# Performance work log

Hardware: AMD Instinct MI355X
Metric: run time of the kernel (lower is better)

## Reference

```python
import jax, jax.numpy as jnp
import numpy as np

N_NODES = 100000
N_EDGES = 3200000
D_IN = 256
HID = 256
N_CLASSES = 40


def setup_inputs() -> dict:
    key = jax.random.key(0)
    k1, k2, k3, k4 = jax.random.split(key, 4)
    x = jax.random.normal(k1, (N_NODES, D_IN), dtype=jnp.float32)
    edge_index = jax.random.randint(k2, (2, N_EDGES), 0, N_NODES, dtype=jnp.int64)
    W1 = jax.random.normal(k3, (D_IN, HID), dtype=jnp.float32) * (1.0 / np.sqrt(D_IN))
    b1 = jnp.zeros((HID,), dtype=jnp.float32)
    W2 = jax.random.normal(k4, (HID, N_CLASSES), dtype=jnp.float32) * (1.0 / np.sqrt(HID))
    b2 = jnp.zeros((N_CLASSES,), dtype=jnp.float32)
    return {"x": x, "edge_index": edge_index, "W1": W1, "b1": b1, "W2": W2, "b2": b2}


def reference(x, edge_index, W1, b1, W2, b2):
    N = x.shape[0]
    loops = jnp.arange(N, dtype=edge_index.dtype)
    # gcn_norm: add self-loops, symmetric normalization D^-1/2 (A+I) D^-1/2
    src = jnp.concatenate([edge_index[0], loops])  # [E+N]
    dst = jnp.concatenate([edge_index[1], loops])
    ew = jnp.ones(src.shape[0], dtype=x.dtype)
    deg = jax.ops.segment_sum(ew, dst, num_segments=N)  # degree at target nodes
    dinv = jnp.where(deg > 0, jax.lax.rsqrt(deg), 0.0).astype(x.dtype)
    norm = dinv[src] * dinv[dst]  # [E+N]

    def propagate(h):
        # out[dst] += norm * h[src]  (SpMM via gather + segment scatter-add)
        return jax.ops.segment_sum(norm[:, None] * h[src], dst, num_segments=N)

    h = propagate(x) @ W1 + b1   # SGConv k=1 + Linear
    h = jax.nn.relu(h)
    h = propagate(h) @ W2 + b2
    return jax.nn.log_softmax(h, axis=1)
```

## Files before the change

kernel.cpp:

```cpp
#include <hip/hip_runtime.h>
#include <hip/hip_bf16.h>

#define N_NODES 100000
#define N_EDGES 3200000
#define D_IN 256
#define HID 256
#define NC 40
#define NBUCK 391
#define CHUNK 8192
#define BIN1_BLOCKS ((N_EDGES + CHUNK - 1) / CHUNK)
#define BCAP 16384
#define NPADE (NBUCK * BCAP)

typedef unsigned short u16;
typedef unsigned int u32;
typedef __attribute__((ext_vector_type(8))) short bf16x8;
typedef __attribute__((ext_vector_type(4))) float f32x4;
typedef __attribute__((ext_vector_type(2))) float f32x2;

static __device__ __forceinline__ float bf2f(u16 u) {
  union { unsigned int i; float f; } c; c.i = ((unsigned int)u) << 16; return c.f;
}
static __device__ __forceinline__ u16 f2bf(float f) {
  union { float f; unsigned int i; } c; c.f = f;
  unsigned int x = c.i;
  x += 0x7fffu + ((x >> 16) & 1u);
  return (u16)(x >> 16);
}

__global__ void k_zero(int* __restrict__ gcur) {
  int i = blockIdx.x * 256 + threadIdx.x;
  if (i < NBUCK) gcur[i] = i * BCAP;
}

__global__ __launch_bounds__(1024) void k_bin1(const int* __restrict__ ei,
    int* __restrict__ gcur, u32* __restrict__ binned) {
  __shared__ int cnt[NBUCK];
  __shared__ int base[NBUCK];
  int t = threadIdx.x;
  int e0 = blockIdx.x * CHUNK;
  for (int j = t; j < NBUCK; j += 1024) cnt[j] = 0;
  __syncthreads();
  for (int j = 0; j < CHUNK / 1024; ++j) {
    int e = e0 + j * 1024 + t;
    if (e < N_EDGES) {
      unsigned d = (unsigned)ei[N_EDGES + e];
      if (d < N_NODES) atomicAdd(&cnt[d >> 8], 1);
    }
  }
  __syncthreads();
  for (int j = t; j < NBUCK; j += 1024)
    base[j] = cnt[j] ? atomicAdd(&gcur[j], cnt[j]) : 0;
  __syncthreads();
  for (int j = 0; j < CHUNK / 1024; ++j) {
    int e = e0 + j * 1024 + t;
    if (e < N_EDGES) {
      unsigned s = (unsigned)ei[e];
      unsigned d = (unsigned)ei[N_EDGES + e];
      if (s < N_NODES && d < N_NODES) {
        int b = d >> 8;
        int pos = atomicAdd(&base[b], 1);
        if ((unsigned)pos < NPADE)
          binned[pos] = ((d & 255u) << 17) | s;
      }
    }
  }
}

__global__ __launch_bounds__(1024) void k_bin2(const u32* __restrict__ binned,
    const int* __restrict__ gcur, int* __restrict__ rp, int* __restrict__ re,
    float* __restrict__ dinv, int* __restrict__ ed) {
  __shared__ int cnt[256];
  __shared__ int s[256];
  __shared__ int cur[256];
  int b = blockIdx.x, t = threadIdx.x;
  int start = b * BCAP, end = gcur[b];
  if (t < 256) cnt[t] = 0;
  __syncthreads();
  for (int i = start + t; i < end; i += 1024)
    atomicAdd(&cnt[binned[i] >> 17], 1);
  __syncthreads();
  int v = (t < 256) ? cnt[t] : 0;
  if (t < 256) s[t] = v;
  __syncthreads();
  for (int off = 1; off < 256; off <<= 1) {
    int add = (t >= off && t < 256) ? s[t - off] : 0;
    __syncthreads();
    if (t < 256) s[t] += add;
    __syncthreads();
  }
  if (t < 256) {
    int excl = s[t] - v;
    int n = b * 256 + t;
    if (n < N_NODES) {
      rp[n] = start + excl;
      re[n] = start + excl + v;
      dinv[n] = rsqrtf((float)v + 1.0f);
    }
    cur[t] = start + excl;
  }
  __syncthreads();
  for (int i = start + t; i < end; i += 1024) {
    u32 rec = binned[i];
    int pos = atomicAdd(&cur[rec >> 17], 1);
    if ((unsigned)pos < NPADE) ed[pos] = (int)(rec & 0x1FFFFu);
  }
}

__global__ void k_w1t(const float* __restrict__ W1, u16* __restrict__ w1t) {
  int n = blockIdx.x, k = threadIdx.x;
  w1t[n * 256 + k] = f2bf(W1[k * 256 + n]);
}
__global__ void k_w2t(const float* __restrict__ W2, u16* __restrict__ w2t) {
  int n = blockIdx.x, k = threadIdx.x;
  w2t[n * 256 + k] = (n < NC) ? f2bf(W2[k * NC + n]) : (u16)0;
}

__global__ __launch_bounds__(256) void k_gemm1(const float* __restrict__ x,
    const u16* __restrict__ w1t, const float* __restrict__ dinv,
    unsigned char* __restrict__ y) {
  __shared__ char smem[20480];
  short* sA = (short*)smem;
  short* sB = (short*)(smem + 10240);
  float* sdinv = (float*)(smem + 18432);
  int tid = threadIdx.x;
  int wave = tid >> 6, lane = tid & 63;
  int lq = lane >> 4, lr = lane & 15;
  int wm = (wave >> 1) * 64, wn = (wave & 1) * 64;
  int row0 = blockIdx.y * 128;
  int col0 = blockIdx.x * 128;
  int sr = tid >> 1;
  int sh = (tid & 1) * 16;
  int arow = row0 + sr;
  bool aval = arow < N_NODES;
  const float* axf = x + (size_t)arow * 256 + sh;
  const u16* bx = w1t + (size_t)(col0 + sr) * 256 + sh;
  f32x4 acc[4][4] = {};
  for (int k0 = 0; k0 < 256; k0 += 32) {
    float4 f0 = {}, f1 = {}, f2 = {}, f3 = {};
    if (aval) {
      f0 = *(const float4*)(axf + k0);
      f1 = *(const float4*)(axf + k0 + 4);
      f2 = *(const float4*)(axf + k0 + 8);
      f3 = *(const float4*)(axf + k0 + 12);
    }
    uint4 vb0 = *(const uint4*)(bx + k0);
    uint4 vb1 = *(const uint4*)(bx + k0 + 8);
    uint4 pa0, pa1;
    pa0.x = (u32)f2bf(f0.x) | ((u32)f2bf(f0.y) << 16);
    pa0.y = (u32)f2bf(f0.z) | ((u32)f2bf(f0.w) << 16);
    pa0.z = (u32)f2bf(f1.x) | ((u32)f2bf(f1.y) << 16);
    pa0.w = (u32)f2bf(f1.z) | ((u32)f2bf(f1.w) << 16);
    pa1.x = (u32)f2bf(f2.x) | ((u32)f2bf(f2.y) << 16);
    pa1.y = (u32)f2bf(f2.z) | ((u32)f2bf(f2.w) << 16);
    pa1.z = (u32)f2bf(f3.x) | ((u32)f2bf(f3.y) << 16);
    pa1.w = (u32)f2bf(f3.z) | ((u32)f2bf(f3.w) << 16);
    __syncthreads();
    *(uint4*)&sA[sr * 40 + sh] = pa0;
    *(uint4*)&sA[sr * 40 + sh + 8] = pa1;
    *(uint4*)&sB[sr * 40 + sh] = vb0;
    *(uint4*)&sB[sr * 40 + sh + 8] = vb1;
    __syncthreads();
    bf16x8 af[4], bfr[4];
#pragma unroll
    for (int mt = 0; mt < 4; ++mt)
      af[mt] = *(const bf16x8*)&sA[(wm + mt * 16 + lr) * 40 + lq * 8];
#pragma unroll
    for (int nt = 0; nt < 4; ++nt)
      bfr[nt] = *(const bf16x8*)&sB[(wn + nt * 16 + lr) * 40 + lq * 8];
#pragma unroll
    for (int mt = 0; mt < 4; ++mt)
#pragma unroll
      for (int nt = 0; nt < 4; ++nt)
        acc[mt][nt] = __builtin_amdgcn_mfma_f32_16x16x32_bf16(
            af[mt], bfr[nt], acc[mt][nt], 0, 0, 0);
  }
  __syncthreads();
  if (tid < 128) {
    int rr = row0 + tid;
    sdinv[tid] = (rr < N_NODES) ? dinv[rr] : 0.f;
  }
  __syncthreads();
#pragma unroll
  for (int mt = 0; mt < 4; ++mt)
#pragma unroll
    for (int nt = 0; nt < 4; ++nt) {
      int c = wn + nt * 16 + lr;
#pragma unroll
      for (int i = 0; i < 4; ++i) {
        int r = wm + mt * 16 + lq * 4 + i;
        float sv = sdinv[r] * acc[mt][nt][i];
        int pk = __builtin_amdgcn_cvt_pk_fp8_f32(sv, sv, 0, false);
        smem[r * 144 + c] = (char)(pk & 0xFF);
      }
    }
  __syncthreads();
  if (aval) {
    unsigned char* dst = y + (size_t)arow * 256 + col0 + (tid & 1) * 64;
    const char* srcp = smem + sr * 144 + (tid & 1) * 64;
#pragma unroll
    for (int j = 0; j < 4; ++j)
      ((uint4*)dst)[j] = *(const uint4*)(srcp + j * 16);
  }
}

#define ACC8(U) do { \
    acc[0] += __builtin_amdgcn_cvt_pk_f32_fp8((U).x, false); \
    acc[1] += __builtin_amdgcn_cvt_pk_f32_fp8((U).x, true);  \
    acc[2] += __builtin_amdgcn_cvt_pk_f32_fp8((U).y, false); \
    acc[3] += __builtin_amdgcn_cvt_pk_f32_fp8((U).y, true);  \
    acc[4] += __builtin_amdgcn_cvt_pk_f32_fp8((U).z, false); \
    acc[5] += __builtin_amdgcn_cvt_pk_f32_fp8((U).z, true);  \
    acc[6] += __builtin_amdgcn_cvt_pk_f32_fp8((U).w, false); \
    acc[7] += __builtin_amdgcn_cvt_pk_f32_fp8((U).w, true);  \
  } while (0)

__global__ __launch_bounds__(256) void k_spmm1(const uint4* __restrict__ y16,
    const int* __restrict__ ed, const int* __restrict__ rp,
    const int* __restrict__ re, const float* __restrict__ dinv,
    const float* __restrict__ b1, u16* __restrict__ h1, int row0) {
  int lane = threadIdx.x & 63;
  int row = row0 + (blockIdx.x << 2) + (threadIdx.x >> 6);
  int g = lane >> 4, p = lane & 15;
  float di = dinv[row];
  uint4 sv = y16[(size_t)row * 16 + p];
  f32x2 acc[8];
  f32x2 z2 = {0.f, 0.f};
  if (g == 0) {
    acc[0] = __builtin_amdgcn_cvt_pk_f32_fp8(sv.x, false);
    acc[1] = __builtin_amdgcn_cvt_pk_f32_fp8(sv.x, true);
    acc[2] = __builtin_amdgcn_cvt_pk_f32_fp8(sv.y, false);
    acc[3] = __builtin_amdgcn_cvt_pk_f32_fp8(sv.y, true);
    acc[4] = __builtin_amdgcn_cvt_pk_f32_fp8(sv.z, false);
    acc[5] = __builtin_amdgcn_cvt_pk_f32_fp8(sv.z, true);
    acc[6] = __builtin_amdgcn_cvt_pk_f32_fp8(sv.w, false);
    acc[7] = __builtin_amdgcn_cvt_pk_f32_fp8(sv.w, true);
  } else {
#pragma unroll
    for (int i = 0; i < 8; ++i) acc[i] = z2;
  }
  int e = rp[row], e1 = re[row];
  if (e + 16 <= e1) {
    int s0 = ed[e + g], s1 = ed[e + 4 + g];
    int s2 = ed[e + 8 + g], s3 = ed[e + 12 + g];
    while (true) {
      uint4 u0 = y16[(size_t)s0 * 16 + p];
      uint4 u1 = y16[(size_t)s1 * 16 + p];
      uint4 u2 = y16[(size_t)s2 * 16 + p];
      uint4 u3 = y16[(size_t)s3 * 16 + p];
      e += 16;
      bool more = (e + 16 <= e1);
      if (more) {
        s0 = ed[e + g]; s1 = ed[e + 4 + g];
        s2 = ed[e + 8 + g]; s3 = ed[e + 12 + g];
      }
      ACC8(u0);
      ACC8(u1);
      ACC8(u2);
      ACC8(u3);
      if (!more) break;
    }
  }
  for (; e + 4 <= e1; e += 4) {
    int s0 = ed[e + g];
    uint4 u0 = y16[(size_t)s0 * 16 + p];
    ACC8(u0);
  }
  int rem = e1 - e;
  if (rem > 0) {
    int s0 = ed[e + (g < rem ? g : 0)];
    uint4 u0 = y16[(size_t)s0 * 16 + p];
    if (g < rem) ACC8(u0);
  }
#pragma unroll
  for (int i = 0; i < 8; ++i) {
    acc[i].x += __shfl_xor(acc[i].x, 16);
    acc[i].y += __shfl_xor(acc[i].y, 16);
    acc[i].x += __shfl_xor(acc[i].x, 32);
    acc[i].y += __shfl_xor(acc[i].y, 32);
  }
  if (g == 0) {
    const float4* bb4 = (const float4*)(b1 + p * 16);
    u16 o[16];
#pragma unroll
    for (int i = 0; i < 4; ++i) {
      float4 bb = bb4[i];
      float a0 = fmaxf(di * acc[2 * i].x + bb.x, 0.f);
      float a1 = fmaxf(di * acc[2 * i].y + bb.y, 0.f);
      float a2 = fmaxf(di * acc[2 * i + 1].x + bb.z, 0.f);
      float a3 = fmaxf(di * acc[2 * i + 1].y + bb.w, 0.f);
      o[4 * i + 0] = f2bf(a0);
      o[4 * i + 1] = f2bf(a1);
      o[4 * i + 2] = f2bf(a2);
      o[4 * i + 3] = f2bf(a3);
    }
    u16* dst = h1 + (size_t)row * HID + p * 16;
    *(uint4*)dst = *(const uint4*)&o[0];
    *(uint4*)(dst + 8) = *(const uint4*)&o[8];
  }
}

__global__ __launch_bounds__(256) void k_gemm2(const u16* __restrict__ h1,
    const u16* __restrict__ w2t, const float* __restrict__ dinv,
    u16* __restrict__ zbp) {
  __shared__ char smem[16384];
  short* sA = (short*)smem;
  short* sB = (short*)(smem + 10240);
  float* sdinv = (float*)(smem + 14336);
  u16* sC = (u16*)smem;
  int tid = threadIdx.x;
  int wave = tid >> 6, lane = tid & 63;
  int lq = lane >> 4, lr = lane & 15;
  int wm = wave * 32;
  int row0 = blockIdx.x * 128;
  int sr = tid >> 1;
  int sh = (tid & 1) * 16;
  int arow = row0 + sr;
  bool aval = arow < N_NODES;
  const u16* ax = h1 + (size_t)arow * 256 + sh;
  int br = tid >> 1;
  const u16* bx = w2t + (size_t)br * 256 + sh;
  if (tid < 128) {
    int rr = row0 + tid;
    sdinv[tid] = (rr < N_NODES) ? dinv[rr] : 0.f;
  }
  f32x4 acc[2][3] = {};
  for (int k0 = 0; k0 < 256; k0 += 32) {
    uint4 a0 = {}, a1 = {};
    if (aval) {
      a0 = *(const uint4*)(ax + k0);
      a1 = *(const uint4*)(ax + k0 + 8);
    }
    uint4 b0 = {}, b1v = {};
    if (tid < 96) {
      b0 = *(const uint4*)(bx + k0);
      b1v = *(const uint4*)(bx + k0 + 8);
    }
    __syncthreads();
    *(uint4*)&sA[sr * 40 + sh] = a0;
    *(uint4*)&sA[sr * 40 + sh + 8] = a1;
    if (tid < 96) {
      *(uint4*)&sB[br * 40 + sh] = b0;
      *(uint4*)&sB[br * 40 + sh + 8] = b1v;
    }
    __syncthreads();
    bf16x8 af[2], bfr[3];
#pragma unroll
    for (int mt = 0; mt < 2; ++mt)
      af[mt] = *(const bf16x8*)&sA[(wm + mt * 16 + lr) * 40 + lq * 8];
#pragma unroll
    for (int nt = 0; nt < 3; ++nt)
      bfr[nt] = *(const bf16x8*)&sB[(nt * 16 + lr) * 40 + lq * 8];
#pragma unroll
    for (int mt = 0; mt < 2; ++mt)
#pragma unroll
      for (int nt = 0; nt < 3; ++nt)
        acc[mt][nt] = __builtin_amdgcn_mfma_f32_16x16x32_bf16(
            af[mt], bfr[nt], acc[mt][nt], 0, 0, 0);
  }
  __syncthreads();
#pragma unroll
  for (int mt = 0; mt < 2; ++mt)
#pragma unroll
    for (int nt = 0; nt < 3; ++nt) {
      int c = nt * 16 + lr;
#pragma unroll
      for (int i = 0; i < 4; ++i) {
        int r = wm + mt * 16 + lq * 4 + i;
        sC[r * 56 + c] = f2bf(sdinv[r] * acc[mt][nt][i]);
      }
    }
  __syncthreads();
  if (tid < 128) {
    int orow = row0 + tid;
    if (orow < N_NODES) {
      u16* dst = zbp + (size_t)orow * 64;
#pragma unroll
      for (int j = 0; j < 6; ++j)
        ((uint4*)dst)[j] = *(const uint4*)&sC[tid * 56 + j * 8];
      uint4 z = {};
      ((uint4*)dst)[6] = z;
      ((uint4*)dst)[7] = z;
    }
  }
}

#define ZACC(U) do { \
    acc[0] += __uint_as_float((U).x << 16); \
    acc[1] += __uint_as_float((U).x & 0xFFFF0000u); \
    acc[2] += __uint_as_float((U).y << 16); \
    acc[3] += __uint_as_float((U).y & 0xFFFF0000u); \
    acc[4] += __uint_as_float((U).z << 16); \
    acc[5] += __uint_as_float((U).z & 0xFFFF0000u); \
    acc[6] += __uint_as_float((U).w << 16); \
    acc[7] += __uint_as_float((U).w & 0xFFFF0000u); \
  } while (0)

__global__ __launch_bounds__(256) void k_spmm2(const uint4* __restrict__ zb4,
    const int* __restrict__ ed, const int* __restrict__ rp,
    const int* __restrict__ re, const float* __restrict__ dinv,
    const float* __restrict__ b2, float* __restrict__ out, int row0) {
  int lane = threadIdx.x & 63;
  int row = row0 + (blockIdx.x << 2) + (threadIdx.x >> 6);
  int g = lane >> 3, p = lane & 7;
  float di = dinv[row];
  float acc[8];
  uint4 sv = zb4[(size_t)row * 8 + p];
  if (g == 0) {
    acc[0] = __uint_as_float(sv.x << 16);
    acc[1] = __uint_as_float(sv.x & 0xFFFF0000u);
    acc[2] = __uint_as_float(sv.y << 16);
    acc[3] = __uint_as_float(sv.y & 0xFFFF0000u);
    acc[4] = __uint_as_float(sv.z << 16);
    acc[5] = __uint_as_float(sv.z & 0xFFFF0000u);
    acc[6] = __uint_as_float(sv.w << 16);
    acc[7] = __uint_as_float(sv.w & 0xFFFF0000u);
  } else {
#pragma unroll
    for (int i = 0; i < 8; ++i) acc[i] = 0.f;
  }
  int e = rp[row], e1 = re[row];
  if (e + 32 <= e1) {
    int s0 = ed[e + g], s1 = ed[e + 8 + g];
    int s2 = ed[e + 16 + g], s3 = ed[e + 24 + g];
    while (true) {
      uint4 u0 = zb4[(size_t)s0 * 8 + p];
      uint4 u1 = zb4[(size_t)s1 * 8 + p];
      uint4 u2 = zb4[(size_t)s2 * 8 + p];
      uint4 u3 = zb4[(size_t)s3 * 8 + p];
      e += 32;
      bool more = (e + 32 <= e1);
      if (more) {
        s0 = ed[e + g]; s1 = ed[e + 8 + g];
        s2 = ed[e + 16 + g]; s3 = ed[e + 24 + g];
      }
      ZACC(u0);
      ZACC(u1);
      ZACC(u2);
      ZACC(u3);
      if (!more) break;
    }
  }
  for (; e + 8 <= e1; e += 8) {
    int s0 = ed[e + g];
    uint4 u0 = zb4[(size_t)s0 * 8 + p];
    ZACC(u0);
  }
  int rem = e1 - e;
  if (g < rem) {
    int s0 = ed[e + g];
    uint4 u0 = zb4[(size_t)s0 * 8 + p];
    ZACC(u0);
  }
#pragma unroll
  for (int i = 0; i < 8; ++i) {
    acc[i] += __shfl_xor(acc[i], 8);
    acc[i] += __shfl_xor(acc[i], 16);
    acc[i] += __shfl_xor(acc[i], 32);
  }
  bool valid = p < 5;
  float val[8];
  if (valid) {
    float4 bb0 = *(const float4*)(b2 + p * 8);
    float4 bb1 = *(const float4*)(b2 + p * 8 + 4);
    val[0] = di * acc[0] + bb0.x;
    val[1] = di * acc[1] + bb0.y;
    val[2] = di * acc[2] + bb0.z;
    val[3] = di * acc[3] + bb0.w;
    val[4] = di * acc[4] + bb1.x;
    val[5] = di * acc[5] + bb1.y;
    val[6] = di * acc[6] + bb1.z;
    val[7] = di * acc[7] + bb1.w;
  } else {
#pragma unroll
    for (int i = 0; i < 8; ++i) val[i] = 0.f;
  }
  float mv = -3.0e38f;
  if (valid) {
#pragma unroll
    for (int i = 0; i < 8; ++i) mv = fmaxf(mv, val[i]);
  }
  mv = fmaxf(mv, __shfl_xor(mv, 1));
  mv = fmaxf(mv, __shfl_xor(mv, 2));
  mv = fmaxf(mv, __shfl_xor(mv, 4));
  float sum = 0.f;
  if (valid) {
#pragma unroll
    for (int i = 0; i < 8; ++i) sum += expf(val[i] - mv);
  }
  sum += __shfl_xor(sum, 1);
  sum += __shfl_xor(sum, 2);
  sum += __shfl_xor(sum, 4);
  float ls = logf(sum);
  if (g == 0 && valid) {
    float4 o0, o1;
    o0.x = val[0] - mv - ls; o0.y = val[1] - mv - ls;
    o0.z = val[2] - mv - ls; o0.w = val[3] - mv - ls;
    o1.x = val[4] - mv - ls; o1.y = val[5] - mv - ls;
    o1.z = val[6] - mv - ls; o1.w = val[7] - mv - ls;
    float* dst = out + (size_t)row * NC + p * 8;
    *(float4*)dst = o0;
    *(float4*)(dst + 4) = o1;
  }
}

extern "C" void kernel_launch(void* const* d_in, const int* in_sizes, int n_in,
                              void* d_out, int out_size, void* d_ws, size_t ws_size,
                              hipStream_t stream) {
  const float* x  = (const float*)d_in[0];
  const int*   ei = (const int*)d_in[1];
  const float* W1 = (const float*)d_in[2];
  const float* b1 = (const float*)d_in[3];
  const float* W2 = (const float*)d_in[4];
  const float* b2 = (const float*)d_in[5];
  float* out = (float*)d_out;

  char* ws = (char*)d_ws;
  size_t off = 0;
  auto alloc = [&](size_t bytes) {
    char* p = ws + off;
    off = (off + bytes + 255) & ~(size_t)255;
    return p;
  };
  int*   gcur   = (int*)  alloc((size_t)NBUCK * 4);
  int*   rp     = (int*)  alloc((size_t)N_NODES * 4);
  int*   re     = (int*)  alloc((size_t)N_NODES * 4);
  float* dinv   = (float*)alloc((size_t)N_NODES * 4);
  u32*   binned = (u32*)  alloc((size_t)NPADE * 4);
  int*   ed     = (int*)  alloc((size_t)NPADE * 4);
  unsigned char* y = (unsigned char*)alloc((size_t)N_NODES * 256);
  u16*   w1t    = (u16*)  alloc((size_t)256 * 256 * 2);
  u16*   w2t    = (u16*)  alloc((size_t)48 * 256 * 2);
  u16*   h1     = (u16*)  alloc((size_t)N_NODES * HID * 2);
  u16*   zbp    = (u16*)  alloc((size_t)N_NODES * 64 * 2);

  k_zero<<<2, 256, 0, stream>>>(gcur);
  k_bin1<<<BIN1_BLOCKS, 1024, 0, stream>>>(ei, gcur, binned);
  k_bin2<<<NBUCK, 1024, 0, stream>>>(binned, gcur, rp, re, dinv, ed);
  k_w1t<<<256, 256, 0, stream>>>(W1, w1t);
  k_w2t<<<48, 256, 0, stream>>>(W2, w2t);
  k_gemm1<<<dim3(2, (N_NODES + 127) / 128), 256, 0, stream>>>(x, w1t, dinv, y);
  k_spmm1<<<N_NODES / 8, 256, 0, stream>>>((const uint4*)y, ed, rp, re, dinv, b1, h1, 0);
  k_spmm1<<<N_NODES / 8, 256, 0, stream>>>((const uint4*)y, ed, rp, re, dinv, b1, h1, N_NODES / 2);
  k_gemm2<<<(N_NODES + 127) / 128, 256, 0, stream>>>(h1, w2t, dinv, zbp);
  k_spmm2<<<N_NODES / 8, 256, 0, stream>>>((const uint4*)zbp, ed, rp, re, dinv, b2, out, 0);
  k_spmm2<<<N_NODES / 8, 256, 0, stream>>>((const uint4*)zbp, ed, rp, re, dinv, b2, out, N_NODES / 2);
}
```

Baseline: 481.3 us.

## Double-buffer LDS in gemm1 with XOR-swizzled layout and packed bf16 conversion

Restructures the first GEMM's main loop to use two LDS buffers, so the next K-slice is loaded and staged while MFMAs run on the current one. This cuts the loop to one barrier per step instead of two. It also replaces the padded row stride with an XOR swizzle to avoid bank conflicts, and uses a packed float2-to-bf16 conversion intrinsic. The dinv load is hoisted before the loop. In exchange, LDS use grows to about 33KB per block, which may reduce occupancy, and GEMM1 is likely only part of the total runtime.

```diff
diff --git a/kernel.cpp b/kernel.cpp
--- a/kernel.cpp
+++ b/kernel.cpp
@@ -26,6 +26,10 @@
   unsigned int x = c.i;
   x += 0x7fffu + ((x >> 16) & 1u);
   return (u16)(x >> 16);
+}
+static __device__ __forceinline__ u32 pkbf(float a, float b) {
+  __hip_bfloat162 t = __float22bfloat162_rn(make_float2(a, b));
+  union { __hip_bfloat162 h; u32 u; } c; c.h = t; return c.u;
 }
 
 __global__ void k_zero(int* __restrict__ gcur) {
@@ -119,10 +123,8 @@
 __global__ __launch_bounds__(256) void k_gemm1(const float* __restrict__ x,
     const u16* __restrict__ w1t, const float* __restrict__ dinv,
     unsigned char* __restrict__ y) {
-  __shared__ char smem[20480];
-  short* sA = (short*)smem;
-  short* sB = (short*)(smem + 10240);
-  float* sdinv = (float*)(smem + 18432);
+  __shared__ char smem[33280];
+  float* sdinv = (float*)(smem + 32768);
   int tid = threadIdx.x;
   int wave = tid >> 6, lane = tid & 63;
   int lq = lane >> 4, lr = lane & 15;
@@ -130,13 +132,27 @@
   int row0 = blockIdx.y * 128;
   int col0 = blockIdx.x * 128;
   int sr = tid >> 1;
-  int sh = (tid & 1) * 16;
+  int h = tid & 1;
+  int sh = h * 16;
   int arow = row0 + sr;
   bool aval = arow < N_NODES;
   const float* axf = x + (size_t)arow * 256 + sh;
   const u16* bx = w1t + (size_t)(col0 + sr) * 256 + sh;
-  f32x4 acc[4][4] = {};
-  for (int k0 = 0; k0 < 256; k0 += 32) {
+  if (tid < 128) {
+    int rr = row0 + tid;
+    sdinv[tid] = (rr < N_NODES) ? dinv[rr] : 0.f;
+  }
+  int wsw0 = sr * 32 + (((2 * h)     ^ ((sr >> 1) & 3)) * 8);
+  int wsw1 = sr * 32 + (((2 * h + 1) ^ ((sr >> 1) & 3)) * 8);
+  int rdo[4], rdb[4];
+#pragma unroll
+  for (int mt = 0; mt < 4; ++mt) {
+    int Ra = wm + mt * 16 + lr;
+    int Rb = wn + mt * 16 + lr;
+    rdo[mt] = Ra * 32 + ((lq ^ ((Ra >> 1) & 3)) * 8);
+    rdb[mt] = Rb * 32 + ((lq ^ ((Rb >> 1) & 3)) * 8);
+  }
+  auto stage = [&](int k0, int boff) {
     float4 f0 = {}, f1 = {}, f2 = {}, f3 = {};
     if (aval) {
       f0 = *(const float4*)(axf + k0);
@@ -147,40 +163,44 @@
     uint4 vb0 = *(const uint4*)(bx + k0);
     uint4 vb1 = *(const uint4*)(bx + k0 + 8);
     uint4 pa0, pa1;
-    pa0.x = (u32)f2bf(f0.x) | ((u32)f2bf(f0.y) << 16);
-    pa0.y = (u32)f2bf(f0.z) | ((u32)f2bf(f0.w) << 16);
-    pa0.z = (u32)f2bf(f1.x) | ((u32)f2bf(f1.y) << 16);
-    pa0.w = (u32)f2bf(f1.z) | ((u32)f2bf(f1.w) << 16);
-    pa1.x = (u32)f2bf(f2.x) | ((u32)f2bf(f2.y) << 16);
-    pa1.y = (u32)f2bf(f2.z) | ((u32)f2bf(f2.w) << 16);
-    pa1.z = (u32)f2bf(f3.x) | ((u32)f2bf(f3.y) << 16);
-    pa1.w = (u32)f2bf(f3.z) | ((u32)f2bf(f3.w) << 16);
-    __syncthreads();
-    *(uint4*)&sA[sr * 40 + sh] = pa0;
-    *(uint4*)&sA[sr * 40 + sh + 8] = pa1;
-    *(uint4*)&sB[sr * 40 + sh] = vb0;
-    *(uint4*)&sB[sr * 40 + sh + 8] = vb1;
-    __syncthreads();
+    pa0.x = pkbf(f0.x, f0.y);
+    pa0.y = pkbf(f0.z, f0.w);
+    pa0.z = pkbf(f1.x, f1.y);
+    pa0.w = pkbf(f1.z, f1.w);
+    pa1.x = pkbf(f2.x, f2.y);
+    pa1.y = pkbf(f2.z, f2.w);
+    pa1.z = pkbf(f3.x, f3.y);
+    pa1.w = pkbf(f3.z, f3.w);
+    short* a = (short*)(smem + boff);
+    short* b = (short*)(smem + boff + 8192);
+    *(uint4*)&a[wsw0] = pa0;
+    *(uint4*)&a[wsw1] = pa1;
+    *(uint4*)&b[wsw0] = vb0;
+    *(uint4*)&b[wsw1] = vb1;
+  };
+  f32x4 acc[4][4] = {};
+  stage(0, 0);
+  __syncthreads();
+#pragma unroll
+  for (int step = 0; step < 8; ++step) {
+    int curb = (step & 1) * 16384;
+    int nxtb = 16384 - curb;
+    if (step < 7) stage((step + 1) * 32, nxtb);
+    const short* a = (const short*)(smem + curb);
+    const short* b = (const short*)(smem + curb + 8192);
     bf16x8 af[4], bfr[4];
 #pragma unroll
-    for (int mt = 0; mt < 4; ++mt)
-      af[mt] = *(const bf16x8*)&sA[(wm + mt * 16 + lr) * 40 + lq * 8];
-#pragma unroll
-    for (int nt = 0; nt < 4; ++nt)
-      bfr[nt] = *(const bf16x8*)&sB[(wn + nt * 16 + lr) * 40 + lq * 8];
+    for (int mt = 0; mt < 4; ++mt) af[mt] = *(const bf16x8*)&a[rdo[mt]];
+#pragma unroll
+    for (int nt = 0; nt < 4; ++nt) bfr[nt] = *(const bf16x8*)&b[rdb[nt]];
 #pragma unroll
     for (int mt = 0; mt < 4; ++mt)
 #pragma unroll
       for (int nt = 0; nt < 4; ++nt)
         acc[mt][nt] = __builtin_amdgcn_mfma_f32_16x16x32_bf16(
             af[mt], bfr[nt], acc[mt][nt], 0, 0, 0);
-  }
-  __syncthreads();
-  if (tid < 128) {
-    int rr = row0 + tid;
-    sdinv[tid] = (rr < N_NODES) ? dinv[rr] : 0.f;
-  }
-  __syncthreads();
+    __syncthreads();
+  }
 #pragma unroll
   for (int mt = 0; mt < 4; ++mt)
 #pragma unroll
@@ -196,8 +216,8 @@
     }
   __syncthreads();
   if (aval) {
-    unsigned char* dst = y + (size_t)arow * 256 + col0 + (tid & 1) * 64;
-    const char* srcp = smem + sr * 144 + (tid & 1) * 64;
+    unsigned char* dst = y + (size_t)arow * 256 + col0 + h * 64;
+    const char* srcp = smem + sr * 144 + h * 64;
 #pragma unroll
     for (int j = 0; j < 4; ++j)
       ((uint4*)dst)[j] = *(const uint4*)(srcp + j * 16);
```

After: 487.1 us. No clear change (+1.2%).
